# Optimization experiments

Measured on AMD Instinct MI355X. Metric: run time of the kernel, lower is better.

The kernel has to match this reference:

```python
import jax, jax.numpy as jnp
import numpy as np

IN_CHANS = 64
OUT_CHANS = 64
IN_SHAPE = (128, 128)
RADIUS_CUTOFF = 0.03
KERNEL_SHAPE = (3, 4)  # (n_rings, n_phi) -> (3-1)*4+1 = 9 basis functions
EPS = 1e-5
NEG_SLOPE = 0.2


def _disco_basis():
    """Dynamically compile the DISCO filter basis on the (2H, 2W) equidistant grid.

    Returns psi of shape [K, kh, kw] (K=9 hat-function basis filters, including
    quadrature weight hx*hy) plus the pixel radii (Ry, Rx) of the support.
    All static -> constant-folded under jit.
    """
    H2, W2 = 2 * IN_SHAPE[0], 2 * IN_SHAPE[1]
    r_cut = RADIUS_CUTOFF / 2.0
    hy, hx = 1.0 / H2, 1.0 / W2            # normalized grid spacing
    Ry = int(np.ceil(r_cut / hy))
    Rx = int(np.ceil(r_cut / hx))
    dy = np.arange(-Ry, Ry + 1)[:, None] * hy
    dx = np.arange(-Rx, Rx + 1)[None, :] * hx
    r = np.sqrt(dy * dy + dx * dx)
    phi = np.arctan2(dy, dx) % (2.0 * np.pi)
    nr, nphi = KERNEL_SHAPE
    K = (nr - 1) * nphi + 1
    dr = r_cut / (nr - 1)
    dphi = 2.0 * np.pi / nphi
    ik = np.arange(K)[:, None, None]
    ir = np.where(ik > 0, (ik - 1) // nphi + 1, 0)   # radial ring index
    iphi = (ik - 1) % nphi                            # angular index
    # radial hat functions centered at ir*dr, clipped at the cutoff radius
    r_val = np.where((np.abs(r - ir * dr) <= dr) & (r <= r_cut),
                     1.0 - np.abs(r - ir * dr) / dr, 0.0)
    # periodic angular hat functions centered at iphi*dphi
    d_ang = np.abs(phi - iphi * dphi)
    d_ang = np.minimum(d_ang, 2.0 * np.pi - d_ang)
    phi_val = np.where(d_ang <= dphi, 1.0 - d_ang / dphi, 0.0)
    psi = np.where(ik == 0, r_val, r_val * phi_val)   # center basis is isotropic
    psi = psi * (hx * hy)                              # quadrature weight
    return jnp.asarray(psi, jnp.float32), Ry, Rx


def _upsample2x_align_corners(x):
    """Bilinear 2x upsample with align_corners=True, x: [N, C, H, W]."""
    N, C, H, W = x.shape

    def axis(n):
        no = 2 * n
        s = jnp.arange(no, dtype=jnp.float32) * (n - 1) / (no - 1)
        i0 = jnp.floor(s).astype(jnp.int32)
        i1 = jnp.minimum(i0 + 1, n - 1)
        w = (s - i0).astype(x.dtype)
        return i0, i1, w

    y0, y1, wy = axis(H)
    x = x[:, :, y0, :] * (1.0 - wy)[None, None, :, None] + x[:, :, y1, :] * wy[None, None, :, None]
    x0, x1, wx = axis(W)
    x = x[:, :, :, x0] * (1.0 - wx) + x[:, :, :, x1] * wx
    return x


def setup_inputs() -> dict:
    key = jax.random.key(0)
    k1, k2 = jax.random.split(key)
    image = jax.random.normal(k1, (4, IN_CHANS, IN_SHAPE[0], IN_SHAPE[1]), dtype=jnp.float32)
    K = (KERNEL_SHAPE[0] - 1) * KERNEL_SHAPE[1] + 1
    scale = 1.0 / np.sqrt(IN_CHANS * K)
    weight = jax.random.normal(k2, (OUT_CHANS, IN_CHANS, K), dtype=jnp.float32) * scale
    return {"image": image, "weight": weight}


def reference(image, weight):
    x = _upsample2x_align_corners(image)  # [N, Cin, 2H, 2W]
    # 2) DISCO conv: contract learned weights with compiled basis -> dense filter
    psi, Ry, Rx = _disco_basis()          # [K, kh, kw]
    kernel = jnp.einsum('oik,khw->oihw', weight, psi)
    y = jax.lax.conv_general_dilated(
        x, kernel, window_strides=(1, 1),
        padding=[(Ry, Ry), (Rx, Rx)],       # 'constant' zero padding, same size
        dimension_numbers=('NCHW', 'OIHW', 'NCHW'))
    # 3) InstanceNorm2d (affine=False, biased variance, eps=1e-5)
    mu = jnp.mean(y, axis=(2, 3), keepdims=True)
    var = jnp.var(y, axis=(2, 3), keepdims=True)
    y = (y - mu) * jax.lax.rsqrt(var + EPS)
    # 4) LeakyReLU(0.2)
    return jnp.where(y >= 0, y, NEG_SLOPE * y)
```

## Files before the change

kernel.cpp:

```cpp
#include <hip/hip_runtime.h>

#define NB 4
#define CIN 64
#define COUT 64
#define H 128
#define W 128
#define H2 256
#define W2 256
#define HSX 23
#define ZS 40

#define WS_W    0
#define WS_P1   32768
#define WS_P2   98304
#define WS_MU   163840
#define WS_RSTD 164096

constexpr double csqrt(double x) {
    double g = x > 1.0 ? x : 1.0;
    for (int i = 0; i < 64; ++i) g = 0.5 * (g + x / g);
    return g;
}
constexpr double catan_pos(double x) {
    double f = 1.0;
    for (int i = 0; i < 6; ++i) { x = x / (1.0 + csqrt(1.0 + x * x)); f *= 2.0; }
    double x2 = x * x, s = 0.0, term = x;
    for (int n = 0; n < 10; ++n) { s += term / (2 * n + 1) * ((n & 1) ? -1.0 : 1.0); term *= x2; }
    return f * s;
}
constexpr double catan2c(double y, double x) {
    const double PI = 3.141592653589793;
    if (x == 0.0 && y == 0.0) return 0.0;
    double ax = x < 0 ? -x : x, ay = y < 0 ? -y : y;
    double a = (ax >= ay) ? catan_pos(ay / ax) : (PI / 2.0 - catan_pos(ax / ay));
    if (x < 0) a = PI - a;
    return (y < 0) ? -a : a;
}

struct PsiTab { double v[81][9]; };
constexpr PsiTab compute_psi() {
    PsiTab P{};
    const double hy = 1.0 / 256.0;
    const double rcut = 0.015;
    const double dr = 0.0075;
    const double PI = 3.141592653589793;
    const double TWO_PI = 6.283185307179586;
    const double dphi = PI / 2.0;
    for (int ky = 0; ky < 9; ++ky)
        for (int kx = 0; kx < 9; ++kx) {
            double dy = (double)(ky - 4) * hy;
            double dx = (double)(kx - 4) * hy;
            double r = csqrt(dy * dy + dx * dx);
            double phi = catan2c(dy, dx);
            if (phi < 0.0) phi += TWO_PI;
            for (int k = 0; k < 9; ++k) {
                int ir = (k == 0) ? 0 : ((k - 1) / 4 + 1);
                double ctr = ir * dr;
                double ad = r > ctr ? r - ctr : ctr - r;
                double rv = (ad <= dr && r <= rcut) ? 1.0 - ad / dr : 0.0;
                double val;
                if (k == 0) val = rv;
                else {
                    int ip = (k - 1) % 4;
                    double da = phi - ip * dphi; if (da < 0) da = -da;
                    double d2 = TWO_PI - da; if (d2 < da) da = d2;
                    double pv = (da <= dphi) ? 1.0 - da / dphi : 0.0;
                    val = rv * pv;
                }
                P.v[ky * 9 + kx][k] = val * (hy * hy);
            }
        }
    return P;
}

struct TapTab {
    int nt;
    int off[48];
    float val[48][9];
    bool nz[48][9];
};
constexpr TapTab make_taps() {
    TapTab T{};
    PsiTab P = compute_psi();
    for (int ky = 0; ky < 9; ++ky)
        for (int kx = 0; kx < 9; ++kx) {
            int t = ky * 9 + kx;
            bool any = false;
            for (int k = 0; k < 9; ++k) if (P.v[t][k] != 0.0) any = true;
            if (!any) continue;
            int dy = ky - 4, dx = kx - 4;
            T.off[T.nt] = dy * HSX + dx;
            for (int k = 0; k < 9; ++k) {
                T.val[T.nt][k] = (float)P.v[t][k];
                T.nz[T.nt][k] = (P.v[t][k] != 0.0);
            }
            T.nt++;
        }
    return T;
}
constexpr TapTab TT = make_taps();
constexpr int NT = TT.nt;
static_assert(NT > 0 && NT <= 48, "tap table overflow");

using f32x2  = __attribute__((ext_vector_type(2))) float;
using f32x4  = __attribute__((ext_vector_type(4))) float;
using bf16x8 = __attribute__((ext_vector_type(8))) short;

__device__ __forceinline__ unsigned short f2bf_rne(float f) {
    unsigned u = __float_as_uint(f);
    unsigned r = (u + 0x7fff + ((u >> 16) & 1)) >> 16;
    return (unsigned short)r;
}
__device__ __forceinline__ unsigned pkrtz(float a, float b) {
    return (__float_as_uint(a) >> 16) | (__float_as_uint(b) & 0xffff0000u);
}

__global__ void setup_w(const float* __restrict__ wgt, float* __restrict__ ws) {
    unsigned short* wsW = (unsigned short*)(ws + WS_W);
    const int g = blockIdx.x;
    const int t = threadIdx.x;
    const int o = t >> 2;
    const int k0 = (t & 3) * 8;
#pragma unroll
    for (int j = 0; j < 8; ++j) {
        int kk = k0 + j;
        int ch = kk >> 4, k = kk & 15;
        float v = (k < 9) ? wgt[((size_t)o * CIN + 2 * g + ch) * 9 + k] : 0.f;
        wsW[g * 2048 + o * 32 + kk] = f2bf_rne(v);
    }
}

__global__ __launch_bounds__(256, 2) void conv_kernel(const float* __restrict__ img,
                                                      float* __restrict__ out,
                                                      float* __restrict__ ws) {
    __shared__ __align__(16) unsigned short zbuf[2][256][ZS];
    __shared__ f32x2 halo[2][22 * HSX];
    __shared__ f32x2 coarse[2][14 * 15];
    __shared__ float red1[4][64], red2[4][64];

    const int tid  = threadIdx.x;
    const int bid  = blockIdx.x;
    const int n    = bid >> 8;
    const int tile = bid & 255;
    const int ty0  = (tile >> 4) << 4;
    const int tx0  = (tile & 15) << 4;

    const int r = tid >> 4, c = tid & 15;
    const int hbase = (r + 3) * HSX + (c + 3);
    const int wv  = tid >> 6;
    const int l   = tid & 63;
    const int a16 = l & 15;
    const int kseg = (l >> 4) * 8;

    const unsigned short* wsW = (const unsigned short*)(ws + WS_W);

    {
        uint4* zr = (uint4*)&zbuf[0][0][0];
#pragma unroll
        for (int j = 0; j < 10; ++j) zr[tid + j * 256] = make_uint4(0, 0, 0, 0);
    }

    const float cs = 0.49803922f;

    int cy0 = (int)floorf((float)(ty0 - 3) * cs); cy0 = min(max(cy0, 0), 114);
    int cx0 = (int)floorf((float)(tx0 - 3) * cs); cx0 = min(max(cx0, 0), 114);

    const bool cok = tid < 196;
    const int ci = tid / 14, cj = tid - ci * 14;
    const int cgoff = (cy0 + ci) * W + (cx0 + cj);
    const int cwidx = ci * 15 + cj;
    float cv0 = 0.f, cv1 = 0.f;

    auto cload = [&](int g) {
        if (cok) {
            const float* b = img + ((size_t)n * CIN + 2 * g) * (H * W) + cgoff;
            cv0 = b[0];
            cv1 = b[H * W];
        }
    };
    auto cwrite = [&](int q) {
        if (cok) coarse[q][cwidx] = (f32x2){cv0, cv1};
    };

    unsigned fM[2];
    float fFY[2], fFX[2];
#pragma unroll
    for (int j = 0; j < 2; ++j) {
        int e = tid + j * 256;
        if (e < 484) {
            int hy = e / 22, hx = e - hy * 22;
            int uy = ty0 - 3 + hy, ux = tx0 - 3 + hx;
            unsigned zf = (((unsigned)uy >= 256u) || ((unsigned)ux >= 256u)) ? 1u : 0u;
            float syf = (float)uy * cs;
            float sxf = (float)ux * cs;
            int y0 = (int)floorf(syf);
            int x0 = (int)floorf(sxf);
            fFY[j] = syf - (float)y0;
            fFX[j] = sxf - (float)x0;
            int y0c = min(max(y0, 0), 127), x0c = min(max(x0, 0), 127);
            int dyo = min(y0c + 1, 127) - y0c;
            int dxo = min(x0c + 1, 127) - x0c;
            unsigned A = (unsigned)((y0c - cy0) * 15 + (x0c - cx0));
            fM[j] = A | ((unsigned)dxo << 9) | ((unsigned)dyo << 10) | (zf << 11)
                      | ((unsigned)(hy * HSX + hx) << 12);
        }
    }

    auto fine_build = [&](int q) {
#pragma unroll
        for (int j = 0; j < 2; ++j)
            if (tid < 484 - j * 256) {
                unsigned m = fM[j];
                const f32x2* cb = &coarse[q][0];
                int A = m & 511;
                int dxo = (m >> 9) & 1;
                int dyo = ((m >> 10) & 1) * 15;
                f32x2 c00 = cb[A],       c01 = cb[A + dxo];
                f32x2 c10 = cb[A + dyo], c11 = cb[A + dyo + dxo];
                f32x2 fyv = (f32x2){fFY[j], fFY[j]};
                f32x2 fxv = (f32x2){fFX[j], fFX[j]};
                f32x2 t0 = c00 + fyv * (c10 - c00);
                f32x2 t1 = c01 + fyv * (c11 - c01);
                f32x2 v  = t0 + fxv * (t1 - t0);
                if (m & (1u << 11)) v = (f32x2){0.f, 0.f};
                halo[q][m >> 12] = v;
            }
    };

    auto zphase = [&](int p) {
        const f32x2* hb = &halo[p][hbase - 72];
        f32x2 z[9];
#pragma unroll
        for (int k = 0; k < 9; ++k) z[k] = (f32x2){0.f, 0.f};
#pragma unroll
        for (int t = 0; t < NT; ++t) {
            f32x2 h = hb[72 + TT.off[t]];
#pragma unroll
            for (int k = 0; k < 9; ++k)
                if (TT.nz[t][k]) z[k] += h * TT.val[t][k];
        }
        unsigned short* zr = &zbuf[p][tid][0];
        *(uint4*)zr = make_uint4(pkrtz(z[0].x, z[1].x), pkrtz(z[2].x, z[3].x),
                                 pkrtz(z[4].x, z[5].x), pkrtz(z[6].x, z[7].x));
        zr[8] = (unsigned short)(__float_as_uint(z[8].x) >> 16);
        *(uint4*)(zr + 16) = make_uint4(pkrtz(z[0].y, z[1].y), pkrtz(z[2].y, z[3].y),
                                        pkrtz(z[4].y, z[5].y), pkrtz(z[6].y, z[7].y));
        zr[24] = (unsigned short)(__float_as_uint(z[8].y) >> 16);
    };

    f32x4 acc[4][4];
#pragma unroll
    for (int m = 0; m < 4; ++m)
#pragma unroll
        for (int t = 0; t < 4; ++t) acc[m][t] = (f32x4){0.f, 0.f, 0.f, 0.f};

    cload(0); cwrite(0);
    __syncthreads();
    fine_build(0);
    cload(1);
    __syncthreads();
    cwrite(1);
    cload(2);
    __syncthreads();

#pragma unroll 1
    for (int i = 0; i <= 32; ++i) {
        if (i >= 1) {
            const int zp = (i - 1) & 1;
            bf16x8 af[4];
            const unsigned short* wp = wsW + (i - 1) * 2048 + a16 * 32 + kseg;
#pragma unroll
            for (int m = 0; m < 4; ++m)
                af[m] = *(const bf16x8*)(wp + m * 512);
            union { uint4 q4; bf16x8 v; } bfr;
#pragma unroll
            for (int t = 0; t < 4; ++t) {
                bfr.q4 = *(const uint4*)&zbuf[zp][wv * 64 + t * 16 + a16][kseg];
#pragma unroll
                for (int m = 0; m < 4; ++m)
                    acc[m][t] = __builtin_amdgcn_mfma_f32_16x16x32_bf16(af[m], bfr.v, acc[m][t], 0, 0, 0);
            }
        }
        if (i < 32)  zphase(i & 1);
        if (i <= 29) cwrite(i & 1);
        if (i <= 30) fine_build((i + 1) & 1);
        if (i <= 28) cload(i + 3);
        __syncthreads();
    }

#pragma unroll
    for (int m = 0; m < 4; ++m) {
#pragma unroll
        for (int r4 = 0; r4 < 4; ++r4) {
            float s = 0.f, q = 0.f;
#pragma unroll
            for (int t = 0; t < 4; ++t) {
                float v = acc[m][t][r4];
                s += v; q = fmaf(v, v, q);
            }
#pragma unroll
            for (int msk = 1; msk < 16; msk <<= 1) {
                s += __shfl_xor(s, msk);
                q += __shfl_xor(q, msk);
            }
            if (a16 == 0) {
                int o = m * 16 + (l >> 4) * 4 + r4;
                red1[wv][o] = s;
                red2[wv][o] = q;
            }
        }
    }

    const size_t nbase = (size_t)n * COUT * (H2 * W2);
#pragma unroll
    for (int m = 0; m < 4; ++m)
#pragma unroll
        for (int t = 0; t < 4; ++t) {
            int Y = ty0 + wv * 4 + t;
            int X = tx0 + a16;
#pragma unroll
            for (int r4 = 0; r4 < 4; ++r4) {
                int o = m * 16 + (l >> 4) * 4 + r4;
                out[nbase + (size_t)o * (H2 * W2) + Y * W2 + X] = acc[m][t][r4];
            }
        }
    __syncthreads();
    if (tid < 64) {
        float S1 = red1[0][tid] + red1[1][tid] + red1[2][tid] + red1[3][tid];
        float S2 = red2[0][tid] + red2[1][tid] + red2[2][tid] + red2[3][tid];
        ws[WS_P1 + (n * COUT + tid) * 256 + tile] = S1;
        ws[WS_P2 + (n * COUT + tid) * 256 + tile] = S2;
    }
}

__global__ void stats_kernel(float* __restrict__ ws) {
    const int co  = blockIdx.x;
    const int tid = threadIdx.x;
    float s1 = ws[WS_P1 + co * 256 + tid];
    float s2 = ws[WS_P2 + co * 256 + tid];
#pragma unroll
    for (int m = 1; m < 64; m <<= 1) { s1 += __shfl_xor(s1, m); s2 += __shfl_xor(s2, m); }
    __shared__ float r1[4], r2[4];
    if ((tid & 63) == 0) { r1[tid >> 6] = s1; r2[tid >> 6] = s2; }
    __syncthreads();
    if (tid == 0) {
        float S1 = r1[0] + r1[1] + r1[2] + r1[3];
        float S2 = r2[0] + r2[1] + r2[2] + r2[3];
        const float inv = 1.f / 65536.f;
        float mu  = S1 * inv;
        float var = S2 * inv - mu * mu;
        ws[WS_MU + co]   = mu;
        ws[WS_RSTD + co] = 1.f / sqrtf(var + 1e-5f);
    }
}

__global__ void norm_kernel(float* __restrict__ out, const float* __restrict__ ws) {
    const int total = NB * COUT * H2 * W2 / 4;
    for (int idx = blockIdx.x * blockDim.x + threadIdx.x; idx < total;
         idx += gridDim.x * blockDim.x) {
        int co = idx >> 14;
        float mu = ws[WS_MU + co];
        float rs = ws[WS_RSTD + co];
        float4 v = ((float4*)out)[idx];
        float* p = (float*)&v;
#pragma unroll
        for (int j = 0; j < 4; ++j) {
            float t = (p[j] - mu) * rs;
            p[j] = (t >= 0.f) ? t : 0.2f * t;
        }
        ((float4*)out)[idx] = v;
    }
}

extern "C" void kernel_launch(void* const* d_in, const int* in_sizes, int n_in,
                              void* d_out, int out_size, void* d_ws, size_t ws_size,
                              hipStream_t stream) {
    const float* img = (const float*)d_in[0];
    const float* wgt = (const float*)d_in[1];
    float* out = (float*)d_out;
    float* ws  = (float*)d_ws;

    setup_w<<<32, 256, 0, stream>>>(wgt, ws);
    conv_kernel<<<NB * 256, 256, 0, stream>>>(img, out, ws);
    stats_kernel<<<256, 256, 0, stream>>>(ws);
    norm_kernel<<<2048, 256, 0, stream>>>(out, ws);
}
```

Baseline: 155.5 us.

## Process four input channels per stage with bf16-packed halo and restructured pipeline

The upsample-to-halo pipeline now handles four input channels per step instead of two. Coarse tiles for channels 0-1 and 2-3 are kept in separate buffers, and the halo stores bf16-packed values in a single buffer instead of f32 double buffers. The main loop runs 16 groups, each with two MFMA steps and two barriers, splitting the z writes so the second pair is written after the first MFMA. This aims to cut per-channel barrier and LDS overhead and shrink shared memory, but it quantizes the halo to bf16 before the basis contraction and changes the overlap schedule.

New measurement: 170.0 us. 1.09x slower.

```diff
diff --git a/kernel.cpp b/kernel.cpp
--- a/kernel.cpp
+++ b/kernel.cpp
@@ -134,8 +134,9 @@
                                                       float* __restrict__ out,
                                                       float* __restrict__ ws) {
     __shared__ __align__(16) unsigned short zbuf[2][256][ZS];
-    __shared__ f32x2 halo[2][22 * HSX];
-    __shared__ f32x2 coarse[2][14 * 15];
+    __shared__ uint2 halo[22 * HSX];
+    __shared__ f32x2 coarse01[14 * 15];
+    __shared__ f32x2 coarse23[14 * 15];
     __shared__ float red1[4][64], red2[4][64];
 
     const int tid  = threadIdx.x;
@@ -169,17 +170,22 @@
     const int ci = tid / 14, cj = tid - ci * 14;
     const int cgoff = (cy0 + ci) * W + (cx0 + cj);
     const int cwidx = ci * 15 + cj;
-    float cv0 = 0.f, cv1 = 0.f;
-
-    auto cload = [&](int g) {
+    float cv0 = 0.f, cv1 = 0.f, cv2 = 0.f, cv3 = 0.f;
+
+    auto cload = [&](int g4) {
         if (cok) {
-            const float* b = img + ((size_t)n * CIN + 2 * g) * (H * W) + cgoff;
+            const float* b = img + ((size_t)n * CIN + 4 * g4) * (H * W) + cgoff;
             cv0 = b[0];
             cv1 = b[H * W];
-        }
-    };
-    auto cwrite = [&](int q) {
-        if (cok) coarse[q][cwidx] = (f32x2){cv0, cv1};
+            cv2 = b[2 * H * W];
+            cv3 = b[3 * H * W];
+        }
+    };
+    auto cwrite = [&]() {
+        if (cok) {
+            coarse01[cwidx] = (f32x2){cv0, cv1};
+            coarse23[cwidx] = (f32x2){cv2, cv3};
+        }
     };
 
     unsigned fM[2];
@@ -206,46 +212,71 @@
         }
     }
 
-    auto fine_build = [&](int q) {
+    auto fine_build = [&]() {
 #pragma unroll
         for (int j = 0; j < 2; ++j)
             if (tid < 484 - j * 256) {
                 unsigned m = fM[j];
-                const f32x2* cb = &coarse[q][0];
                 int A = m & 511;
                 int dxo = (m >> 9) & 1;
                 int dyo = ((m >> 10) & 1) * 15;
-                f32x2 c00 = cb[A],       c01 = cb[A + dxo];
-                f32x2 c10 = cb[A + dyo], c11 = cb[A + dyo + dxo];
                 f32x2 fyv = (f32x2){fFY[j], fFY[j]};
                 f32x2 fxv = (f32x2){fFX[j], fFX[j]};
-                f32x2 t0 = c00 + fyv * (c10 - c00);
-                f32x2 t1 = c01 + fyv * (c11 - c01);
-                f32x2 v  = t0 + fxv * (t1 - t0);
-                if (m & (1u << 11)) v = (f32x2){0.f, 0.f};
-                halo[q][m >> 12] = v;
-            }
-    };
-
-    auto zphase = [&](int p) {
-        const f32x2* hb = &halo[p][hbase - 72];
-        f32x2 z[9];
-#pragma unroll
-        for (int k = 0; k < 9; ++k) z[k] = (f32x2){0.f, 0.f};
+                f32x2 a00 = coarse01[A],       a01 = coarse01[A + dxo];
+                f32x2 a10 = coarse01[A + dyo], a11 = coarse01[A + dyo + dxo];
+                f32x2 t0 = a00 + fyv * (a10 - a00);
+                f32x2 t1 = a01 + fyv * (a11 - a01);
+                f32x2 v01 = t0 + fxv * (t1 - t0);
+                f32x2 b00 = coarse23[A],       b01 = coarse23[A + dxo];
+                f32x2 b10 = coarse23[A + dyo], b11 = coarse23[A + dyo + dxo];
+                f32x2 u0 = b00 + fyv * (b10 - b00);
+                f32x2 u1 = b01 + fyv * (b11 - b01);
+                f32x2 v23 = u0 + fxv * (u1 - u0);
+                if (m & (1u << 11)) { v01 = (f32x2){0.f, 0.f}; v23 = (f32x2){0.f, 0.f}; }
+                halo[m >> 12] = make_uint2(
+                    (unsigned)f2bf_rne(v01.x) | ((unsigned)f2bf_rne(v01.y) << 16),
+                    (unsigned)f2bf_rne(v23.x) | ((unsigned)f2bf_rne(v23.y) << 16));
+            }
+    };
+
+    f32x2 z23[9];
+
+    auto zphase4 = [&]() {
+        const uint2* hb = &halo[hbase - 72];
+        f32x2 z01[9];
+#pragma unroll
+        for (int k = 0; k < 9; ++k) { z01[k] = (f32x2){0.f, 0.f}; z23[k] = (f32x2){0.f, 0.f}; }
 #pragma unroll
         for (int t = 0; t < NT; ++t) {
-            f32x2 h = hb[72 + TT.off[t]];
+            uint2 d = hb[72 + TT.off[t]];
+            f32x2 h01, h23;
+            h01.x = __uint_as_float(d.x << 16);
+            h01.y = __uint_as_float(d.x & 0xffff0000u);
+            h23.x = __uint_as_float(d.y << 16);
+            h23.y = __uint_as_float(d.y & 0xffff0000u);
 #pragma unroll
             for (int k = 0; k < 9; ++k)
-                if (TT.nz[t][k]) z[k] += h * TT.val[t][k];
-        }
-        unsigned short* zr = &zbuf[p][tid][0];
-        *(uint4*)zr = make_uint4(pkrtz(z[0].x, z[1].x), pkrtz(z[2].x, z[3].x),
-                                 pkrtz(z[4].x, z[5].x), pkrtz(z[6].x, z[7].x));
-        zr[8] = (unsigned short)(__float_as_uint(z[8].x) >> 16);
-        *(uint4*)(zr + 16) = make_uint4(pkrtz(z[0].y, z[1].y), pkrtz(z[2].y, z[3].y),
-                                        pkrtz(z[4].y, z[5].y), pkrtz(z[6].y, z[7].y));
-        zr[24] = (unsigned short)(__float_as_uint(z[8].y) >> 16);
+                if (TT.nz[t][k]) {
+                    z01[k] += h01 * TT.val[t][k];
+                    z23[k] += h23 * TT.val[t][k];
+                }
+        }
+        unsigned short* zr = &zbuf[0][tid][0];
+        *(uint4*)zr = make_uint4(pkrtz(z01[0].x, z01[1].x), pkrtz(z01[2].x, z01[3].x),
+                                 pkrtz(z01[4].x, z01[5].x), pkrtz(z01[6].x, z01[7].x));
+        zr[8] = (unsigned short)(__float_as_uint(z01[8].x) >> 16);
+        *(uint4*)(zr + 16) = make_uint4(pkrtz(z01[0].y, z01[1].y), pkrtz(z01[2].y, z01[3].y),
+                                        pkrtz(z01[4].y, z01[5].y), pkrtz(z01[6].y, z01[7].y));
+        zr[24] = (unsigned short)(__float_as_uint(z01[8].y) >> 16);
+    };
+    auto writez23 = [&]() {
+        unsigned short* zr = &zbuf[1][tid][0];
+        *(uint4*)zr = make_uint4(pkrtz(z23[0].x, z23[1].x), pkrtz(z23[2].x, z23[3].x),
+                                 pkrtz(z23[4].x, z23[5].x), pkrtz(z23[6].x, z23[7].x));
+        zr[8] = (unsigned short)(__float_as_uint(z23[8].x) >> 16);
+        *(uint4*)(zr + 16) = make_uint4(pkrtz(z23[0].y, z23[1].y), pkrtz(z23[2].y, z23[3].y),
+                                        pkrtz(z23[4].y, z23[5].y), pkrtz(z23[6].y, z23[7].y));
+        zr[24] = (unsigned short)(__float_as_uint(z23[8].y) >> 16);
     };
 
     f32x4 acc[4][4];
@@ -254,39 +285,41 @@
 #pragma unroll
         for (int t = 0; t < 4; ++t) acc[m][t] = (f32x4){0.f, 0.f, 0.f, 0.f};
 
-    cload(0); cwrite(0);
+    auto mfma_step = [&](int j) {
+        const int zp = j & 1;
+        bf16x8 af[4];
+        const unsigned short* wp = wsW + j * 2048 + a16 * 32 + kseg;
+#pragma unroll
+        for (int m = 0; m < 4; ++m)
+            af[m] = *(const bf16x8*)(wp + m * 512);
+        union { uint4 q4; bf16x8 v; } bfr;
+#pragma unroll
+        for (int t = 0; t < 4; ++t) {
+            bfr.q4 = *(const uint4*)&zbuf[zp][wv * 64 + t * 16 + a16][kseg];
+#pragma unroll
+            for (int m = 0; m < 4; ++m)
+                acc[m][t] = __builtin_amdgcn_mfma_f32_16x16x32_bf16(af[m], bfr.v, acc[m][t], 0, 0, 0);
+        }
+    };
+
+    cload(0); cwrite();
     __syncthreads();
-    fine_build(0);
-    cload(1);
+    fine_build();
     __syncthreads();
-    cwrite(1);
-    cload(2);
-    __syncthreads();
 
 #pragma unroll 1
-    for (int i = 0; i <= 32; ++i) {
-        if (i >= 1) {
-            const int zp = (i - 1) & 1;
-            bf16x8 af[4];
-            const unsigned short* wp = wsW + (i - 1) * 2048 + a16 * 32 + kseg;
-#pragma unroll
-            for (int m = 0; m < 4; ++m)
-                af[m] = *(const bf16x8*)(wp + m * 512);
-            union { uint4 q4; bf16x8 v; } bfr;
-#pragma unroll
-            for (int t = 0; t < 4; ++t) {
-                bfr.q4 = *(const uint4*)&zbuf[zp][wv * 64 + t * 16 + a16][kseg];
-#pragma unroll
-                for (int m = 0; m < 4; ++m)
-                    acc[m][t] = __builtin_amdgcn_mfma_f32_16x16x32_bf16(af[m], bfr.v, acc[m][t], 0, 0, 0);
-            }
-        }
-        if (i < 32)  zphase(i & 1);
-        if (i <= 29) cwrite(i & 1);
-        if (i <= 30) fine_build((i + 1) & 1);
-        if (i <= 28) cload(i + 3);
+    for (int g = 0; g < 16; ++g) {
+        if (g > 0) mfma_step(2 * g - 1);
+        if (g < 15) cload(g + 1);
+        zphase4();
+        if (g < 15) cwrite();
         __syncthreads();
-    }
+        mfma_step(2 * g);
+        writez23();
+        if (g < 15) fine_build();
+        __syncthreads();
+    }
+    mfma_step(31);
 
 #pragma unroll
     for (int m = 0; m < 4; ++m) {
```
